# Kernel tuning notes

Hardware: AMD Instinct MI355X
Metric: run time of the kernel (lower is better)

The kernel has to match this reference:

```python
import jax, jax.numpy as jnp
import numpy as np

# Hard-coded model hyperparams (RuntimeParams)
B, L, H, NH, FF, DEPTH = 256, 256, 128, 8, 512, 4
PEAK, NCAT, CVOC, KMAX, NNUM, NDIM, TSLOT = 500000, 8, 50001, 8, 4, 32, 256
SCALE = (H // NH) ** -0.5


def _ln(x, g, b):
    m = x.mean(-1, keepdims=True)
    v = ((x - m) ** 2).mean(-1, keepdims=True)
    return (x - m) / jnp.sqrt(v + 1e-5) * g + b


def _block(x, mask, p):
    ln1_g, ln1_b, qw, qb, ow, ob, w1, b1, w2, b2, ln2_g, ln2_b = p
    b, n, c = x.shape
    src = _ln(x, ln1_g, ln1_b)
    qkv = (src @ qw + qb).reshape(b, n, 3, NH, c // NH).transpose(2, 0, 3, 1, 4)
    q, k, v = qkv[0], qkv[1], qkv[2]  # [b, nh, n, dh]
    dots = jnp.einsum('bhid,bhjd->bhij', q, k) * SCALE
    dots = jnp.where(mask[:, None, None, :], dots, -jnp.inf)
    attn = jax.nn.softmax(dots, axis=-1)
    out = jnp.einsum('bhij,bhjd->bhid', attn, v).transpose(0, 2, 1, 3).reshape(b, n, c)
    x = x + out @ ow + ob
    h = _ln(x, ln2_g, ln2_b)
    h = jax.nn.gelu(h @ w1 + b1, approximate=False) @ w2 + b2
    return x + h


def _encode(cat_vals, cat_lens, num_arr, cat_tables, num_W):
    # Vectorized form of the per-sample _encode_fields python loop:
    # per categorical field: mean of embeddings over the ragged value list
    # per numeric field: bias-free linear projection; then mean over all fields.
    emb = cat_tables[jnp.arange(NCAT)[None, :, None], cat_vals]  # [B,F,K,H]
    pos = (jnp.arange(KMAX)[None, None, :] < cat_lens[:, :, None]).astype(emb.dtype)
    fc = (emb * pos[..., None]).sum(2) / cat_lens[:, :, None].astype(emb.dtype)  # [B,F,H]
    fn = jnp.einsum('bfd,fdh->bfh', num_arr, num_W)  # [B,Fn,H]
    return (fc.sum(1) + fn.sum(1)) / (NCAT + NNUM)  # mean over all fields


def setup_inputs() -> dict:
    key = jax.random.key(0)
    ks = iter(jax.random.split(key, 40))
    nk = lambda: next(ks)
    d = {}
    d['item_seq'] = jax.random.randint(nk(), (B, L), 0, PEAK + 5)
    d['action_seq'] = jax.random.randint(nk(), (B, L), 0, 5)
    d['time_diff'] = jax.random.randint(nk(), (B, L), 0, TSLOT)
    seq_lens = jax.random.randint(nk(), (B,), L // 2, L + 1)
    d['mask'] = jnp.arange(L)[None, :] < seq_lens[:, None]
    for pre in ('u', 'i'):
        vals = jax.random.randint(nk(), (B, NCAT, KMAX), 1, CVOC)
        lens = jax.random.randint(nk(), (B, NCAT), 1, KMAX + 1)
        vals = jnp.where(jnp.arange(KMAX)[None, None, :] < lens[:, :, None], vals, 0)
        d[pre + '_cat_vals'] = vals
        d[pre + '_cat_lens'] = lens
        d[pre + '_num'] = jax.random.normal(nk(), (B, NNUM, NDIM), dtype=jnp.float32)
    s = 0.02
    d['item_table'] = (jax.random.normal(nk(), (PEAK + 5, H), dtype=jnp.float32) * s).at[0].set(0.0)
    d['act_table'] = jax.random.normal(nk(), (5, H), dtype=jnp.float32) * s
    d['time_table'] = jax.random.normal(nk(), (TSLOT, H), dtype=jnp.float32) * s
    d['cat_tables'] = (jax.random.normal(nk(), (NCAT, CVOC, H), dtype=jnp.float32) * s).at[:, 0, :].set(0.0)
    d['num_W'] = jax.random.normal(nk(), (NNUM, NDIM, H), dtype=jnp.float32) * s
    d['global_token'] = jax.random.normal(nk(), (1, 1, H), dtype=jnp.float32)
    d['ln1_g'] = jnp.ones((DEPTH, H)); d['ln1_b'] = jnp.zeros((DEPTH, H))
    d['qkv_w'] = jax.random.normal(nk(), (DEPTH, H, 3 * H), dtype=jnp.float32) * s
    d['qkv_b'] = jnp.zeros((DEPTH, 3 * H))
    d['out_w'] = jax.random.normal(nk(), (DEPTH, H, H), dtype=jnp.float32) * s
    d['out_b'] = jnp.zeros((DEPTH, H))
    d['mlp_w1'] = jax.random.normal(nk(), (DEPTH, H, FF), dtype=jnp.float32) * s
    d['mlp_b1'] = jnp.zeros((DEPTH, FF))
    d['mlp_w2'] = jax.random.normal(nk(), (DEPTH, FF, H), dtype=jnp.float32) * s
    d['mlp_b2'] = jnp.zeros((DEPTH, H))
    d['ln2_g'] = jnp.ones((DEPTH, H)); d['ln2_b'] = jnp.zeros((DEPTH, H))
    d['bott_w'] = jax.random.normal(nk(), (H, H), dtype=jnp.float32) * s
    d['bott_b'] = jnp.zeros((H,))
    d['cls_w'] = jax.random.normal(nk(), (H, 1), dtype=jnp.float32) * s
    d['cls_b'] = jnp.zeros((1,))
    return d


def reference(item_seq, action_seq, time_diff, mask, u_cat_vals, u_cat_lens, u_num,
              i_cat_vals, i_cat_lens, i_num, item_table, act_table, time_table,
              cat_tables, num_W, global_token, ln1_g, ln1_b, qkv_w, qkv_b,
              out_w, out_b, mlp_w1, mlp_b1, mlp_w2, mlp_b2, ln2_g, ln2_b,
              bott_w, bott_b, cls_w, cls_b):
    b = item_seq.shape[0]
    seq_feat = item_table[item_seq] + act_table[action_seq] + time_table[time_diff]  # [B,L,H]
    u = _encode(u_cat_vals, u_cat_lens, u_num, cat_tables, num_W)[:, None, :]
    i = _encode(i_cat_vals, i_cat_lens, i_num, cat_tables, num_W)[:, None, :]
    cls = jnp.broadcast_to(global_token, (b, 1, H))
    x = jnp.concatenate([cls, u, i, seq_feat], axis=1)  # [B, 3+L, H]
    fmask = jnp.concatenate([jnp.ones((b, 3), dtype=bool), mask], axis=1)
    for dd in range(DEPTH):
        p = (ln1_g[dd], ln1_b[dd], qkv_w[dd], qkv_b[dd], out_w[dd], out_b[dd],
             mlp_w1[dd], mlp_b1[dd], mlp_w2[dd], mlp_b2[dd], ln2_g[dd], ln2_b[dd])
        x = _block(x, fmask, p)
    latent = x[:, 0, :]
    logits = (jax.nn.relu(latent @ bott_w + bott_b) @ cls_w + cls_b)[:, 0]
    embed = latent / jnp.maximum(jnp.linalg.norm(latent, axis=-1, keepdims=True), 1e-12)
    return logits, embed
```

## Files before the change

### kernel.cpp

```cpp
#include <hip/hip_runtime.h>
#include <cstdio>

#define BATCH 256
#define SEQL 256
#define NPOS 259
#define TTOK (BATCH*NPOS)
#define HD 128
#define NHEAD 8
#define FF 512
#define DEPTH 4
#define CVOC 50001

typedef unsigned short u16;
typedef unsigned int u32;
typedef __bf16 bf16x8 __attribute__((ext_vector_type(8)));
typedef float f32x4 __attribute__((ext_vector_type(4)));
typedef float f32x16 __attribute__((ext_vector_type(16)));

typedef const __attribute__((address_space(1))) u32 gas_u32;
typedef __attribute__((address_space(3))) u32 las_u32;
#define GLOAD16(gptr, lptr) \
  __builtin_amdgcn_global_load_lds((gas_u32*)(gptr), (las_u32*)(lptr), 16, 0, 0)

#define QSCALE 0.36067376022224085f

__device__ __forceinline__ u16 f2bf(float f) {
  u32 i = __float_as_uint(f);
  u32 r = (i + 0x7FFFu + ((i >> 16) & 1u)) >> 16;
  return (u16)r;
}

__global__ void k_transpose_all(const float* __restrict__ qkv_w, const float* __restrict__ out_w,
                                const float* __restrict__ w1, const float* __restrict__ w2,
                                u16* __restrict__ wT) {
  int idx = blockIdx.x * 256 + threadIdx.x;
  const float* in; int K, N, local;
  if (idx < 196608)      { in = qkv_w; K = 128; N = 384; local = idx; }
  else if (idx < 262144) { in = out_w; K = 128; N = 128; local = idx - 196608; }
  else if (idx < 524288) { in = w1;    K = 128; N = 512; local = idx - 262144; }
  else if (idx < 786432) { in = w2;    K = 512; N = 128; local = idx - 524288; }
  else return;
  int k = local % K; int rem = local / K; int n = rem % N; int d = rem / N;
  wT[idx] = f2bf(in[(d * K + k) * N + n]);
}

__global__ __launch_bounds__(128)
void k_build(const int* __restrict__ item_seq, const int* __restrict__ act_seq,
             const int* __restrict__ tdiff,
             const int* __restrict__ ucv, const int* __restrict__ ucl, const float* __restrict__ unum,
             const int* __restrict__ icv, const int* __restrict__ icl, const float* __restrict__ inum,
             const float* __restrict__ item_t, const float* __restrict__ act_t,
             const float* __restrict__ time_t, const float* __restrict__ cat_t,
             const float* __restrict__ numW, const float* __restrict__ gtok,
             const float* __restrict__ g, const float* __restrict__ be,
             float* __restrict__ x, u16* __restrict__ src) {
  int pos = blockIdx.x, b = blockIdx.y, h = threadIdx.x;
  float v;
  if (pos == 0) {
    v = gtok[h];
  } else if (pos <= 2) {
    const int* cv = (pos == 1) ? ucv : icv;
    const int* cl = (pos == 1) ? ucl : icl;
    const float* nm = (pos == 1) ? unum : inum;
    float acc = 0.f;
    for (int f = 0; f < 8; ++f) {
      float s = 0.f;
      for (int k = 0; k < 8; ++k) {
        int idx = cv[(b * 8 + f) * 8 + k];
        s += cat_t[((size_t)f * CVOC + idx) * HD + h];
      }
      acc += s / (float)cl[b * 8 + f];
    }
    for (int f = 0; f < 4; ++f)
      for (int d = 0; d < 32; ++d)
        acc += nm[(b * 4 + f) * 32 + d] * numW[(f * 32 + d) * HD + h];
    v = acc * (1.f / 12.f);
  } else {
    int l = pos - 3;
    v = item_t[(size_t)item_seq[b * SEQL + l] * HD + h]
      + act_t[(size_t)act_seq[b * SEQL + l] * HD + h]
      + time_t[(size_t)tdiff[b * SEQL + l] * HD + h];
  }
  size_t t = (size_t)b * NPOS + pos;
  x[t * HD + h] = v;
  __shared__ float red[2][2];
  float s = v, s2 = v * v;
  #pragma unroll
  for (int o = 32; o; o >>= 1) { s += __shfl_xor(s, o); s2 += __shfl_xor(s2, o); }
  if ((h & 63) == 0) { red[h >> 6][0] = s; red[h >> 6][1] = s2; }
  __syncthreads();
  float S = red[0][0] + red[1][0], S2 = red[0][1] + red[1][1];
  float mean = S * (1.f / HD);
  float rstd = rsqrtf(S2 * (1.f / HD) - mean * mean + 1e-5f);
  src[t * HD + h] = f2bf((v - mean) * rstd * g[h] + be[h]);
}

template <int ACT, bool QS>
__global__ __launch_bounds__(256)
void k_gemm(const u16* __restrict__ X, const u16* __restrict__ WT,
            const float* __restrict__ bias, u16* __restrict__ outp,
            int K, int N) {
  __shared__ __align__(16) u16 lA[128 * 32];
  __shared__ __align__(16) u16 lB[128 * 32];
  const int tid = threadIdx.x;
  const int wave = tid >> 6, lane = tid & 63;
  const int row0 = blockIdx.x * 128;
  const int n0 = blockIdx.y * 128;
  const int wr = (wave >> 1) * 64, wc = (wave & 1) * 64;
  const int sr = lane >> 2;
  const int sc = ((lane & 3) ^ ((lane >> 3) & 3)) << 3;
  const u16* gA0 = X  + (size_t)(row0 + wave * 16 + sr) * K + sc;
  const u16* gA1 = X  + (size_t)(row0 + 64 + wave * 16 + sr) * K + sc;
  const u16* gB0 = WT + (size_t)(n0 + wave * 16 + sr) * K + sc;
  const u16* gB1 = WT + (size_t)(n0 + 64 + wave * 16 + sr) * K + sc;
  u16* lA0 = &lA[wave * 512];
  u16* lA1 = &lA[2048 + wave * 512];
  u16* lB0 = &lB[wave * 512];
  u16* lB1 = &lB[2048 + wave * 512];
  const int q = lane & 15;
  const int cg = lane >> 4;
  const int rdoff = ((cg ^ ((q >> 1) & 3)) << 3);
  f32x4 acc[4][4] = {};
  for (int k0 = 0; k0 < K; k0 += 32) {
    __syncthreads();
    GLOAD16(gA0 + k0, lA0);
    GLOAD16(gA1 + k0, lA1);
    GLOAD16(gB0 + k0, lB0);
    GLOAD16(gB1 + k0, lB1);
    __syncthreads();
    bf16x8 af[4], bf[4];
    #pragma unroll
    for (int i = 0; i < 4; ++i)
      af[i] = *(const bf16x8*)&lA[(wr + i * 16 + q) * 32 + rdoff];
    #pragma unroll
    for (int j = 0; j < 4; ++j)
      bf[j] = *(const bf16x8*)&lB[(wc + j * 16 + q) * 32 + rdoff];
    #pragma unroll
    for (int i = 0; i < 4; ++i)
      #pragma unroll
      for (int j = 0; j < 4; ++j)
        acc[i][j] = __builtin_amdgcn_mfma_f32_16x16x32_bf16(af[i], bf[j], acc[i][j], 0, 0, 0);
  }
  const int rg4 = cg * 4;
  #pragma unroll
  for (int i = 0; i < 4; ++i) {
    #pragma unroll
    for (int j = 0; j < 4; ++j) {
      int col = n0 + wc + j * 16 + q;
      float bv = bias[col];
      float scl = (QS && col < 128) ? QSCALE : 1.f;
      #pragma unroll
      for (int jj = 0; jj < 4; ++jj) {
        int row = row0 + wr + i * 16 + rg4 + jj;
        float v = acc[i][j][jj] + bv;
        if (ACT == 1) v = 0.5f * v * (1.f + erff(v * 0.70710678118654752f));
        if (QS) v *= scl;
        outp[(size_t)row * N + col] = f2bf(v);
      }
    }
  }
}

__global__ __launch_bounds__(256)
void k_gemm_ln(const u16* __restrict__ X, const u16* __restrict__ WT,
               const float* __restrict__ bias, float* __restrict__ xio,
               const float* __restrict__ g, const float* __restrict__ be,
               u16* __restrict__ srcout, int K) {
  __shared__ __align__(16) u16 lA[128 * 32];
  __shared__ __align__(16) u16 lB[128 * 32];
  __shared__ float part[128][2][2];
  const int tid = threadIdx.x;
  const int wave = tid >> 6, lane = tid & 63;
  const int row0 = blockIdx.x * 128;
  const int wr = (wave >> 1) * 64, wc = (wave & 1) * 64;
  const int whalf = wave & 1;
  const int sr = lane >> 2;
  const int sc = ((lane & 3) ^ ((lane >> 3) & 3)) << 3;
  const u16* gA0 = X  + (size_t)(row0 + wave * 16 + sr) * K + sc;
  const u16* gA1 = X  + (size_t)(row0 + 64 + wave * 16 + sr) * K + sc;
  const u16* gB0 = WT + (size_t)(wave * 16 + sr) * K + sc;
  const u16* gB1 = WT + (size_t)(64 + wave * 16 + sr) * K + sc;
  u16* lA0 = &lA[wave * 512];
  u16* lA1 = &lA[2048 + wave * 512];
  u16* lB0 = &lB[wave * 512];
  u16* lB1 = &lB[2048 + wave * 512];
  const int q = lane & 15;
  const int cg = lane >> 4;
  const int rdoff = ((cg ^ ((q >> 1) & 3)) << 3);
  f32x4 acc[4][4] = {};
  for (int k0 = 0; k0 < K; k0 += 32) {
    __syncthreads();
    GLOAD16(gA0 + k0, lA0);
    GLOAD16(gA1 + k0, lA1);
    GLOAD16(gB0 + k0, lB0);
    GLOAD16(gB1 + k0, lB1);
    __syncthreads();
    bf16x8 af[4], bf[4];
    #pragma unroll
    for (int i = 0; i < 4; ++i)
      af[i] = *(const bf16x8*)&lA[(wr + i * 16 + q) * 32 + rdoff];
    #pragma unroll
    for (int j = 0; j < 4; ++j)
      bf[j] = *(const bf16x8*)&lB[(wc + j * 16 + q) * 32 + rdoff];
    #pragma unroll
    for (int i = 0; i < 4; ++i)
      #pragma unroll
      for (int j = 0; j < 4; ++j)
        acc[i][j] = __builtin_amdgcn_mfma_f32_16x16x32_bf16(af[i], bf[j], acc[i][j], 0, 0, 0);
  }
  const int rg4 = cg * 4;
  float ps[4][4], ps2[4][4];
  #pragma unroll
  for (int i = 0; i < 4; ++i)
    #pragma unroll
    for (int jj = 0; jj < 4; ++jj) { ps[i][jj] = 0.f; ps2[i][jj] = 0.f; }
  #pragma unroll
  for (int i = 0; i < 4; ++i) {
    #pragma unroll
    for (int j = 0; j < 4; ++j) {
      int col = wc + j * 16 + q;
      float bv = bias[col];
      #pragma unroll
      for (int jj = 0; jj < 4; ++jj) {
        int row = row0 + wr + i * 16 + rg4 + jj;
        float xv = xio[(size_t)row * 128 + col] + acc[i][j][jj] + bv;
        acc[i][j][jj] = xv;
        ps[i][jj] += xv;
        ps2[i][jj] += xv * xv;
      }
    }
  }
  #pragma unroll
  for (int o = 1; o < 16; o <<= 1) {
    #pragma unroll
    for (int i = 0; i < 4; ++i)
      #pragma unroll
      for (int jj = 0; jj < 4; ++jj) {
        ps[i][jj]  += __shfl_xor(ps[i][jj], o);
        ps2[i][jj] += __shfl_xor(ps2[i][jj], o);
      }
  }
  if (q == 0) {
    #pragma unroll
    for (int i = 0; i < 4; ++i)
      #pragma unroll
      for (int jj = 0; jj < 4; ++jj) {
        int rl = wr + i * 16 + rg4 + jj;
        part[rl][whalf][0] = ps[i][jj];
        part[rl][whalf][1] = ps2[i][jj];
      }
  }
  __syncthreads();
  #pragma unroll
  for (int i = 0; i < 4; ++i) {
    #pragma unroll
    for (int jj = 0; jj < 4; ++jj) {
      int rl = wr + i * 16 + rg4 + jj;
      float S  = part[rl][0][0] + part[rl][1][0];
      float S2 = part[rl][0][1] + part[rl][1][1];
      float mean = S * (1.f / 128.f);
      float rstd = rsqrtf(S2 * (1.f / 128.f) - mean * mean + 1e-5f);
      int row = row0 + rl;
      #pragma unroll
      for (int j = 0; j < 4; ++j) {
        int col = wc + j * 16 + q;
        float xv = acc[i][j][jj];
        xio[(size_t)row * 128 + col] = xv;
        srcout[(size_t)row * 128 + col] = f2bf((xv - mean) * rstd * g[col] + be[col]);
      }
    }
  }
}

#define VSTR2 296
__global__ __launch_bounds__(576)
void k_attn(const u16* __restrict__ qkv, const int* __restrict__ mask,
            u16* __restrict__ out) {
  int h = blockIdx.x, b = blockIdx.y;
  __shared__ __align__(16) u16 Klin[9 * 512];
  __shared__ __align__(16) u16 Vt[16 * VSTR2];
  __shared__ int part[4];
  const int tid = threadIdx.x;
  if (tid < 256) {
    int mv = (mask[b * SEQL + tid] != 0) ? 1 : 0;
    #pragma unroll
    for (int o = 32; o; o >>= 1) mv += __shfl_xor(mv, o);
    if ((tid & 63) == 0) part[tid >> 6] = mv;
  }
  {
    int r = tid >> 1, h2 = tid & 1;
    uint4 val = make_uint4(0, 0, 0, 0);
    if (r < NPOS)
      val = *(const uint4*)&qkv[((size_t)(b * NPOS + r)) * 384 + h * 16 + 128 + h2 * 8];
    *(uint4*)&Klin[(r >> 5) * 512 + h2 * 256 + (r & 31) * 8] = val;
  }
  if (tid < 288) {
    int r = tid;
    u16 tmp[16];
    if (r < NPOS) {
      const u16* vp = &qkv[((size_t)(b * NPOS + r)) * 384 + h * 16 + 256];
      *(uint4*)&tmp[0] = *(const uint4*)&vp[0];
      *(uint4*)&tmp[8] = *(const uint4*)&vp[8];
    } else {
      #pragma unroll
      for (int d = 0; d < 16; ++d) tmp[d] = 0;
    }
    #pragma unroll
    for (int d = 0; d < 16; ++d) Vt[d * VSTR2 + r] = tmp[d];
  }
  __syncthreads();
  const int nvalid = part[0] + part[1] + part[2] + part[3] + 3;
  const int ktiles = (nvalid + 31) >> 5;
  const int wave = tid >> 6, lane = tid & 63;
  const int q5 = lane & 31, hi = lane >> 5;
  const f32x16 zf = {};
  const int qt = wave;
  int qrow = qt * 32 + q5;
  int qr = (qrow < NPOS) ? qrow : (NPOS - 1);
  bf16x8 qf = *(const bf16x8*)&qkv[((size_t)(b * NPOS + qr)) * 384 + h * 16 + hi * 8];
  float m = -1e30f, l = 0.f;
  f32x16 acc = {};
  for (int kt = 0; kt < ktiles; ++kt) {
    bf16x8 kf = *(const bf16x8*)&Klin[kt * 512 + lane * 8];
    __builtin_amdgcn_s_setprio(1);
    f32x16 s4 = __builtin_amdgcn_mfma_f32_32x32x16_bf16(kf, qf, zf, 0, 0, 0);
    __builtin_amdgcn_s_setprio(0);
    float p[16];
    float tmax = -1e30f;
    #pragma unroll
    for (int r = 0; r < 16; ++r) {
      int kr = kt * 32 + (r & 3) + 8 * (r >> 2) + 4 * hi;
      float v = (kr < nvalid) ? s4[r] : -1e30f;
      p[r] = v;
      tmax = fmaxf(tmax, v);
    }
    tmax = fmaxf(tmax, __shfl_xor(tmax, 32));
    float mnew = fmaxf(m, tmax);
    float fac = exp2f(m - mnew);
    float tsum = 0.f;
    #pragma unroll
    for (int r = 0; r < 16; ++r) { p[r] = exp2f(p[r] - mnew); tsum += p[r]; }
    tsum += __shfl_xor(tsum, 32);
    l = l * fac + tsum;
    m = mnew;
    #pragma unroll
    for (int r = 0; r < 8; ++r) acc[r] *= fac;
    u32 w[8], xw[8];
    #pragma unroll
    for (int i = 0; i < 8; ++i)
      asm("v_cvt_pk_bf16_f32 %0, %1, %2" : "=v"(w[i]) : "v"(p[2 * i]), "v"(p[2 * i + 1]));
    #pragma unroll
    for (int i = 0; i < 8; ++i) xw[i] = (u32)__shfl_xor((int)w[i], 32);
    union { u32 u[4]; bf16x8 v; } f1, f2;
    if (hi) {
      f1.u[0] = xw[2]; f1.u[1] = xw[3]; f1.u[2] = w[2]; f1.u[3] = w[3];
      f2.u[0] = xw[6]; f2.u[1] = xw[7]; f2.u[2] = w[6]; f2.u[3] = w[7];
    } else {
      f1.u[0] = w[0]; f1.u[1] = w[1]; f1.u[2] = xw[0]; f1.u[3] = xw[1];
      f2.u[0] = w[4]; f2.u[1] = w[5]; f2.u[2] = xw[4]; f2.u[3] = xw[5];
    }
    bf16x8 vf0 = {}, vf1 = {};
    if (q5 < 16) {
      vf0 = *(const bf16x8*)&Vt[q5 * VSTR2 + kt * 32 + hi * 8];
      vf1 = *(const bf16x8*)&Vt[q5 * VSTR2 + kt * 32 + 16 + hi * 8];
    }
    __builtin_amdgcn_s_setprio(1);
    acc = __builtin_amdgcn_mfma_f32_32x32x16_bf16(vf0, f1.v, acc, 0, 0, 0);
    acc = __builtin_amdgcn_mfma_f32_32x32x16_bf16(vf1, f2.v, acc, 0, 0, 0);
    __builtin_amdgcn_s_setprio(0);
  }
  if (qrow < NPOS) {
    float linv = 1.f / l;
    u16* op = &out[((size_t)(b * NPOS + qrow)) * HD + h * 16];
    u32 w0 = (u32)f2bf(acc[0] * linv) | ((u32)f2bf(acc[1] * linv) << 16);
    u32 w1 = (u32)f2bf(acc[2] * linv) | ((u32)f2bf(acc[3] * linv) << 16);
    u32 w2 = (u32)f2bf(acc[4] * linv) | ((u32)f2bf(acc[5] * linv) << 16);
    u32 w3 = (u32)f2bf(acc[6] * linv) | ((u32)f2bf(acc[7] * linv) << 16);
    *(uint2*)&op[4 * hi] = make_uint2(w0, w1);
    *(uint2*)&op[8 + 4 * hi] = make_uint2(w2, w3);
  }
}

__global__ __launch_bounds__(128)
void k_head(const float* __restrict__ x, const float* __restrict__ bw,
            const float* __restrict__ bb, const float* __restrict__ cw,
            const float* __restrict__ cb, float* __restrict__ dout) {
  int b = blockIdx.x, n = threadIdx.x;
  __shared__ float lat[HD];
  __shared__ float redp[2], redss[2];
  float lv = x[((size_t)b * NPOS) * HD + n];
  lat[n] = lv;
  __syncthreads();
  float t = 0.f;
  for (int k = 0; k < HD; ++k) t += lat[k] * bw[k * HD + n];
  t += bb[n];
  t = fmaxf(t, 0.f);
  float p = t * cw[n];
  float ss = lv * lv;
  #pragma unroll
  for (int o = 32; o; o >>= 1) { p += __shfl_xor(p, o); ss += __shfl_xor(ss, o); }
  if ((n & 63) == 0) { redp[n >> 6] = p; redss[n >> 6] = ss; }
  __syncthreads();
  float psum = redp[0] + redp[1];
  float ssum = redss[0] + redss[1];
  if (n == 0) dout[b] = psum + cb[0];
  float nrm = fmaxf(sqrtf(ssum), 1e-12f);
  dout[256 + (size_t)b * HD + n] = lv / nrm;
}

extern "C" void kernel_launch(void* const* d_in, const int* in_sizes, int n_in,
                              void* d_out, int out_size, void* d_ws, size_t ws_size,
                              hipStream_t stream) {
  const int* item_seq = (const int*)d_in[0];
  const int* action_seq = (const int*)d_in[1];
  const int* time_diff = (const int*)d_in[2];
  const int* mask = (const int*)d_in[3];
  const int* u_cv = (const int*)d_in[4];
  const int* u_cl = (const int*)d_in[5];
  const float* u_num = (const float*)d_in[6];
  const int* i_cv = (const int*)d_in[7];
  const int* i_cl = (const int*)d_in[8];
  const float* i_num = (const float*)d_in[9];
  const float* item_t = (const float*)d_in[10];
  const float* act_t = (const float*)d_in[11];
  const float* time_t = (const float*)d_in[12];
  const float* cat_t = (const float*)d_in[13];
  const float* num_W = (const float*)d_in[14];
  const float* gtok = (const float*)d_in[15];
  const float* ln1_g = (const float*)d_in[16];
  const float* ln1_b = (const float*)d_in[17];
  const float* qkv_w = (const float*)d_in[18];
  const float* qkv_b = (const float*)d_in[19];
  const float* out_w = (const float*)d_in[20];
  const float* out_b = (const float*)d_in[21];
  const float* w1 = (const float*)d_in[22];
  const float* b1 = (const float*)d_in[23];
  const float* w2 = (const float*)d_in[24];
  const float* b2 = (const float*)d_in[25];
  const float* ln2_g = (const float*)d_in[26];
  const float* ln2_b = (const float*)d_in[27];
  const float* bott_w = (const float*)d_in[28];
  const float* bott_b = (const float*)d_in[29];
  const float* cls_w = (const float*)d_in[30];
  const float* cls_b = (const float*)d_in[31];

  const size_t off_x   = 0;
  const size_t off_src = 33947648;
  const size_t off_big = 50921472;
  const size_t off_wT  = 118816768;
  const size_t need    = 120389632;
  if (ws_size < need) {
    fprintf(stderr, "kernel_launch: ws_size %zu < needed %zu\n", ws_size, need);
    return;
  }
  char* ws = (char*)d_ws;
  float* x   = (float*)(ws + off_x);
  u16* src   = (u16*)(ws + off_src);
  u16* big   = (u16*)(ws + off_big);
  u16* wT    = (u16*)(ws + off_wT);
  u16* qkvT  = wT;
  u16* outT  = wT + 196608;
  u16* w1T   = wT + 262144;
  u16* w2T   = wT + 524288;

  k_transpose_all<<<3072, 256, 0, stream>>>(qkv_w, out_w, w1, w2, wT);

  k_build<<<dim3(NPOS, BATCH), 128, 0, stream>>>(
      item_seq, action_seq, time_diff, u_cv, u_cl, u_num, i_cv, i_cl, i_num,
      item_t, act_t, time_t, cat_t, num_W, gtok, ln1_g, ln1_b, x, src);

  const int rt = TTOK / 128;
  for (int dd = 0; dd < DEPTH; ++dd) {
    k_gemm<0, true><<<dim3(rt, 3), 256, 0, stream>>>(
        src, qkvT + dd * 49152, qkv_b + dd * 384, big, 128, 384);
    k_attn<<<dim3(NHEAD, BATCH), 576, 0, stream>>>(big, mask, src);
    k_gemm_ln<<<dim3(rt, 1), 256, 0, stream>>>(
        src, outT + dd * 16384, out_b + dd * HD, x,
        ln2_g + dd * HD, ln2_b + dd * HD, src, 128);
    k_gemm<1, false><<<dim3(rt, 4), 256, 0, stream>>>(
        src, w1T + dd * 65536, b1 + dd * FF, big, 128, 512);
    const float* ng = (dd < 3) ? (ln1_g + (dd + 1) * HD) : (ln1_g + dd * HD);
    const float* nb = (dd < 3) ? (ln1_b + (dd + 1) * HD) : (ln1_b + dd * HD);
    k_gemm_ln<<<dim3(rt, 1), 256, 0, stream>>>(
        big, w2T + dd * 65536, b2 + dd * HD, x, ng, nb, src, 512);
  }

  k_head<<<BATCH, 128, 0, stream>>>(x, bott_w, bott_b, cls_w, cls_b, (float*)d_out);
}
```

Measured before the change: 806.8 us.

## Keep A tile resident in LDS and loop over N chunks in GEMM

```diff
diff --git a/kernel.cpp b/kernel.cpp
--- a/kernel.cpp
+++ b/kernel.cpp
@@ -95,67 +95,70 @@
   src[t * HD + h] = f2bf((v - mean) * rstd * g[h] + be[h]);
 }
 
-template <int ACT, bool QS>
+template <int NCH, int ACT, bool QS>
 __global__ __launch_bounds__(256)
-void k_gemm(const u16* __restrict__ X, const u16* __restrict__ WT,
-            const float* __restrict__ bias, u16* __restrict__ outp,
-            int K, int N) {
-  __shared__ __align__(16) u16 lA[128 * 32];
+void k_gemm_nres(const u16* __restrict__ X, const u16* __restrict__ WT,
+                 const float* __restrict__ bias, u16* __restrict__ outp) {
+  const int K = 128, N = NCH * 128;
+  __shared__ __align__(16) u16 lA[4][128 * 32];
   __shared__ __align__(16) u16 lB[128 * 32];
   const int tid = threadIdx.x;
   const int wave = tid >> 6, lane = tid & 63;
   const int row0 = blockIdx.x * 128;
-  const int n0 = blockIdx.y * 128;
   const int wr = (wave >> 1) * 64, wc = (wave & 1) * 64;
   const int sr = lane >> 2;
   const int sc = ((lane & 3) ^ ((lane >> 3) & 3)) << 3;
-  const u16* gA0 = X  + (size_t)(row0 + wave * 16 + sr) * K + sc;
-  const u16* gA1 = X  + (size_t)(row0 + 64 + wave * 16 + sr) * K + sc;
-  const u16* gB0 = WT + (size_t)(n0 + wave * 16 + sr) * K + sc;
-  const u16* gB1 = WT + (size_t)(n0 + 64 + wave * 16 + sr) * K + sc;
-  u16* lA0 = &lA[wave * 512];
-  u16* lA1 = &lA[2048 + wave * 512];
-  u16* lB0 = &lB[wave * 512];
-  u16* lB1 = &lB[2048 + wave * 512];
   const int q = lane & 15;
   const int cg = lane >> 4;
   const int rdoff = ((cg ^ ((q >> 1) & 3)) << 3);
-  f32x4 acc[4][4] = {};
-  for (int k0 = 0; k0 < K; k0 += 32) {
-    __syncthreads();
-    GLOAD16(gA0 + k0, lA0);
-    GLOAD16(gA1 + k0, lA1);
-    GLOAD16(gB0 + k0, lB0);
-    GLOAD16(gB1 + k0, lB1);
-    __syncthreads();
-    bf16x8 af[4], bf[4];
-    #pragma unroll
-    for (int i = 0; i < 4; ++i)
-      af[i] = *(const bf16x8*)&lA[(wr + i * 16 + q) * 32 + rdoff];
-    #pragma unroll
-    for (int j = 0; j < 4; ++j)
-      bf[j] = *(const bf16x8*)&lB[(wc + j * 16 + q) * 32 + rdoff];
-    #pragma unroll
-    for (int i = 0; i < 4; ++i)
+  #pragma unroll
+  for (int s = 0; s < 8; ++s) {
+    int kt = s & 3, rg = 2 * wave + (s >> 2);
+    int r = rg * 16 + sr;
+    GLOAD16(X + (size_t)(row0 + r) * K + kt * 32 + sc, &lA[kt][rg * 512]);
+  }
+  const u16* gB0 = WT + (size_t)(wave * 16 + sr) * K + sc;
+  const u16* gB1 = WT + (size_t)(64 + wave * 16 + sr) * K + sc;
+  u16* lB0 = &lB[wave * 512];
+  u16* lB1 = &lB[2048 + wave * 512];
+  for (int nc = 0; nc < NCH; ++nc) {
+    const size_t nbase = (size_t)nc * 128 * K;
+    f32x4 acc[4][4] = {};
+    for (int k0 = 0; k0 < K; k0 += 32) {
+      __syncthreads();
+      GLOAD16(gB0 + nbase + k0, lB0);
+      GLOAD16(gB1 + nbase + k0, lB1);
+      __syncthreads();
+      const int kt = k0 >> 5;
+      bf16x8 af[4], bf[4];
+      #pragma unroll
+      for (int i = 0; i < 4; ++i)
+        af[i] = *(const bf16x8*)&lA[kt][(wr + i * 16 + q) * 32 + rdoff];
       #pragma unroll
       for (int j = 0; j < 4; ++j)
-        acc[i][j] = __builtin_amdgcn_mfma_f32_16x16x32_bf16(af[i], bf[j], acc[i][j], 0, 0, 0);
-  }
-  const int rg4 = cg * 4;
-  #pragma unroll
-  for (int i = 0; i < 4; ++i) {
-    #pragma unroll
-    for (int j = 0; j < 4; ++j) {
-      int col = n0 + wc + j * 16 + q;
-      float bv = bias[col];
-      float scl = (QS && col < 128) ? QSCALE : 1.f;
-      #pragma unroll
-      for (int jj = 0; jj < 4; ++jj) {
-        int row = row0 + wr + i * 16 + rg4 + jj;
-        float v = acc[i][j][jj] + bv;
-        if (ACT == 1) v = 0.5f * v * (1.f + erff(v * 0.70710678118654752f));
-        if (QS) v *= scl;
-        outp[(size_t)row * N + col] = f2bf(v);
+        bf[j] = *(const bf16x8*)&lB[(wc + j * 16 + q) * 32 + rdoff];
+      #pragma unroll
+      for (int i = 0; i < 4; ++i)
+        #pragma unroll
+        for (int j = 0; j < 4; ++j)
+          acc[i][j] = __builtin_amdgcn_mfma_f32_16x16x32_bf16(af[i], bf[j], acc[i][j], 0, 0, 0);
+    }
+    const int rg4 = cg * 4;
+    const float scl = (QS && nc == 0) ? QSCALE : 1.f;
+    #pragma unroll
+    for (int i = 0; i < 4; ++i) {
+      #pragma unroll
+      for (int j = 0; j < 4; ++j) {
+        int col = nc * 128 + wc + j * 16 + q;
+        float bv = bias[col];
+        #pragma unroll
+        for (int jj = 0; jj < 4; ++jj) {
+          int row = row0 + wr + i * 16 + rg4 + jj;
+          float v = acc[i][j][jj] + bv;
+          if (ACT == 1) v = 0.5f * v * (1.f + erff(v * 0.70710678118654752f));
+          if (QS) v *= scl;
+          outp[(size_t)row * N + col] = f2bf(v);
+        }
       }
     }
   }
@@ -471,14 +474,14 @@
 
   const int rt = TTOK / 128;
   for (int dd = 0; dd < DEPTH; ++dd) {
-    k_gemm<0, true><<<dim3(rt, 3), 256, 0, stream>>>(
-        src, qkvT + dd * 49152, qkv_b + dd * 384, big, 128, 384);
+    k_gemm_nres<3, 0, true><<<rt, 256, 0, stream>>>(
+        src, qkvT + dd * 49152, qkv_b + dd * 384, big);
     k_attn<<<dim3(NHEAD, BATCH), 576, 0, stream>>>(big, mask, src);
     k_gemm_ln<<<dim3(rt, 1), 256, 0, stream>>>(
         src, outT + dd * 16384, out_b + dd * HD, x,
         ln2_g + dd * HD, ln2_b + dd * HD, src, 128);
-    k_gemm<1, false><<<dim3(rt, 4), 256, 0, stream>>>(
-        src, w1T + dd * 65536, b1 + dd * FF, big, 128, 512);
+    k_gemm_nres<4, 1, false><<<rt, 256, 0, stream>>>(
+        src, w1T + dd * 65536, b1 + dd * FF, big);
     const float* ng = (dd < 3) ? (ln1_g + (dd + 1) * HD) : (ln1_g + dd * HD);
     const float* nb = (dd < 3) ? (ln1_b + (dd + 1) * HD) : (ln1_b + dd * HD);
     k_gemm_ln<<<dim3(rt, 1), 256, 0, stream>>>(
```

Result: faster. 784.8 us (-2.7%).
